# Kernel optimization log

Hardware: AMD Instinct MI355X
Metric: run time of the kernel (lower is better)

Reference implementation:

```python
import jax, jax.numpy as jnp
import numpy as np

K = 20  # number of top neighbors kept per row
NOISE_SCALE = 1e-4


def setup_inputs() -> dict:
    key = jax.random.key(0)
    k1, k2 = jax.random.split(key)
    B, N = 16, 2048
    A = jax.random.normal(k1, (B, N, N), dtype=jnp.float32)
    noise = jax.random.uniform(k2, (B, N, N), dtype=jnp.float32)
    return {"A": A, "noise": noise}


def reference(A, noise):
    # _activate: ReLU
    A = jax.nn.relu(A)

    # _sparsify: per-row top-k on noise-doped scores, scatter a 0/1 mask, multiply
    A_doped = A + noise * NOISE_SCALE
    _, topk_idx = jax.lax.top_k(A_doped, K)  # (B, N, K)
    B, N, _ = A.shape
    b_idx = jnp.arange(B)[:, None, None]
    r_idx = jnp.arange(N)[None, :, None]
    mask = jnp.zeros_like(A).at[b_idx, r_idx, topk_idx].set(1.0)
    A = A * mask

    # _symmetrize
    A = (A + jnp.swapaxes(A, 1, 2)) * 0.5

    # _normalize ('sym'): A <- D^{-1/2} (A + I) D^{-1/2}
    A = A + jnp.eye(N, dtype=A.dtype)
    d_inv = jnp.sum(A, axis=2) ** -0.5  # (B, N)
    d_inv = jnp.where(jnp.isinf(d_inv), 0.0, d_inv)
    # diag(d) @ A @ diag(d) expressed via broadcasting (same math as batched matmul)
    A = d_inv[:, :, None] * A * d_inv[:, None, :]
    return A
```

## Files before the change

### kernel.cpp

```cpp
#include <hip/hip_runtime.h>

#define NN 2048
#define KK 20
#define BB 16
#define T0F 1.8f
#define CAP 128
#define CSLOT 64

__global__ __launch_bounds__(256) void topk_kernel(
    const float* __restrict__ A, const float* __restrict__ noise,
    int* __restrict__ sel_idx, float* __restrict__ sel_val,
    float* __restrict__ colsum, int* __restrict__ col_cnt,
    unsigned short* __restrict__ col_src)
{
    __shared__ float cand_key[4][CAP];
    __shared__ float cand_val[4][CAP];
    __shared__ int   cand_idx[4][CAP];
    __shared__ int   tie_idx[4][64];
    __shared__ int   tie_cnt[4];

    const int lane = threadIdx.x & 63;
    const int wv   = threadIdx.x >> 6;
    const int row  = blockIdx.x * 4 + wv;
    const float* Ar = A     + (size_t)row * NN;
    const float* Nr = noise + (size_t)row * NN;
    const int colbase = row & ~(NN - 1);
    const unsigned long long ltm = (1ull << lane) - 1ull;

    int*   si = sel_idx + (size_t)row * KK;
    float* sv = sel_val + (size_t)row * KK;

    float key[32], val[32];
#pragma unroll
    for (int c = 0; c < 8; ++c) {
        float4 a4 = *(const float4*)(Ar + c * 256 + lane * 4);
        float4 n4 = *(const float4*)(Nr + c * 256 + lane * 4);
        val[c*4+0] = fmaxf(a4.x, 0.f); key[c*4+0] = val[c*4+0] + n4.x * 1e-4f;
        val[c*4+1] = fmaxf(a4.y, 0.f); key[c*4+1] = val[c*4+1] + n4.y * 1e-4f;
        val[c*4+2] = fmaxf(a4.z, 0.f); key[c*4+2] = val[c*4+2] + n4.z * 1e-4f;
        val[c*4+3] = fmaxf(a4.w, 0.f); key[c*4+3] = val[c*4+3] + n4.w * 1e-4f;
    }

#define EMIT(POS, IDX, V)                                                      \
    do {                                                                       \
        int _p = (POS); int _i = (IDX); float _v = (V);                        \
        si[_p] = _i; sv[_p] = _v;                                              \
        atomicAdd(&colsum[colbase + _i], _v);                                  \
        int _s = atomicAdd(&col_cnt[colbase + _i], 1);                         \
        if (_s < CSLOT)                                                        \
            col_src[(size_t)(colbase + _i) * CSLOT + _s] =                     \
                (unsigned short)(((row & (NN - 1)) << 5) | _p);                \
    } while (0)

    int cnt = 0;
#pragma unroll
    for (int j = 0; j < 32; ++j) {
        bool p = key[j] >= T0F;
        unsigned long long m = __ballot(p);
        if (p) {
            int pos = cnt + __popcll(m & ltm);
            if (pos < CAP) {
                cand_key[wv][pos] = key[j];
                cand_val[wv][pos] = val[j];
                cand_idx[wv][pos] = (j >> 2) * 256 + lane * 4 + (j & 3);
            }
        }
        cnt += __popcll(m);
    }

    bool done = false;
    if (cnt == KK) {
        if (lane < KK)
            EMIT(lane, cand_idx[wv][lane], cand_val[wv][lane]);
        done = true;
    } else if (cnt > KK && cnt <= CAP) {
        float c0 = (lane      < cnt) ? cand_key[wv][lane]      : -1.f;
        float c1 = (lane + 64 < cnt) ? cand_key[wv][lane + 64] : -1.f;

        float mx = fmaxf(c0, c1);
#pragma unroll
        for (int s = 32; s; s >>= 1) mx = fmaxf(mx, __shfl_xor(mx, s));

        unsigned lo = __float_as_uint(T0F);
        unsigned hi = __float_as_uint(mx) + 1u;
        bool exact = false; unsigned tb = 0;
        while (hi - lo > 1u) {
            unsigned mid = (lo + hi) >> 1;
            float tm = __uint_as_float(mid);
            int c = __popcll(__ballot(c0 >= tm)) + __popcll(__ballot(c1 >= tm));
            if (c == KK) { tb = mid; exact = true; break; }
            if (c > KK) lo = mid; else hi = mid;
        }
        if (exact) {
            float t = __uint_as_float(tb);
            bool p = c0 >= t;
            unsigned long long m = __ballot(p);
            if (p) EMIT(__popcll(m & ltm), cand_idx[wv][lane], cand_val[wv][lane]);
            int run = __popcll(m);
            p = c1 >= t;
            m = __ballot(p);
            if (p) EMIT(run + __popcll(m & ltm), cand_idx[wv][lane + 64],
                        cand_val[wv][lane + 64]);
            done = true;
        }
    }

    if (!done) {
        unsigned lo = 0u, hi = 0x7F800000u;
        unsigned tb = 0u;
        bool exact = false;
        while (hi - lo > 1u) {
            unsigned mid = (lo + hi) >> 1;
            float tm = __uint_as_float(mid);
            int c = 0;
#pragma unroll
            for (int j = 0; j < 32; ++j)
                c += __popcll(__ballot(key[j] >= tm));
            if (c == KK) { tb = mid; exact = true; break; }
            if (c > KK) lo = mid; else hi = mid;
        }
        if (exact) {
            float t = __uint_as_float(tb);
            int run = 0;
#pragma unroll
            for (int j = 0; j < 32; ++j) {
                bool p = key[j] >= t;
                unsigned long long m = __ballot(p);
                if (p) {
                    int pos = run + __popcll(m & ltm);
                    EMIT(pos, (j >> 2) * 256 + lane * 4 + (j & 3), val[j]);
                }
                run += __popcll(m);
            }
        } else {
            float t1 = __uint_as_float(lo);
            int run = 0;
#pragma unroll
            for (int j = 0; j < 32; ++j) {
                bool p = key[j] > t1;
                unsigned long long m = __ballot(p);
                if (p) {
                    int pos = run + __popcll(m & ltm);
                    EMIT(pos, (j >> 2) * 256 + lane * 4 + (j & 3), val[j]);
                }
                run += __popcll(m);
            }
            if (lane == 0) tie_cnt[wv] = 0;
#pragma unroll
            for (int j = 0; j < 32; ++j) {
                if (key[j] == t1) {
                    int p = atomicAdd(&tie_cnt[wv], 1);
                    if (p < 64) tie_idx[wv][p] = (j >> 2) * 256 + lane * 4 + (j & 3);
                }
            }
            if (lane == 0) {
                int n = tie_cnt[wv]; if (n > 64) n = 64;
                int need = KK - run;
                for (int s = 0; s < need; ++s) {
                    int bq = 0, bidx = 0x7fffffff;
                    for (int q = 0; q < n; ++q) {
                        int v = tie_idx[wv][q];
                        if (v < bidx) { bidx = v; bq = q; }
                    }
                    tie_idx[wv][bq] = 0x7fffffff;
                    float v = fmaxf(Ar[bidx], 0.f);
                    EMIT(run + s, bidx, v);
                }
            }
        }
    }
#undef EMIT
}

__global__ __launch_bounds__(256) void dinv_kernel(
    const float* __restrict__ sel_val, const float* __restrict__ colsum,
    float* __restrict__ dinv)
{
    int r = blockIdx.x * 256 + threadIdx.x;
    const float* svp = sel_val + (size_t)r * KK;
    float rs = 0.f;
#pragma unroll
    for (int k = 0; k < KK; ++k) rs += svp[k];
    float d = 1.0f + 0.5f * (rs + colsum[r]);
    dinv[r] = 1.0f / sqrtf(d);
}

__global__ __launch_bounds__(256) void dense_row_kernel(
    const int* __restrict__ sel_idx, const float* __restrict__ sel_val,
    const int* __restrict__ col_cnt, const unsigned short* __restrict__ col_src,
    const float* __restrict__ dinv, float* __restrict__ out)
{
    __shared__ float rowbuf[NN];
    const int r = blockIdx.x;
    const int i = r & (NN - 1);
    const int t = threadIdx.x;
    const int colbase = r & ~(NN - 1);

    float4 z = {0.f, 0.f, 0.f, 0.f};
#pragma unroll
    for (int c = 0; c < 2; ++c)
        *(float4*)(rowbuf + c * 1024 + t * 4) = z;
    __syncthreads();

    float di = dinv[r];
    if (t == 0) atomicAdd(&rowbuf[i], di * di);
    if (t < KK) {
        int j  = sel_idx[(size_t)r * KK + t];
        float v = sel_val[(size_t)r * KK + t];
        atomicAdd(&rowbuf[j], 0.5f * v * di * dinv[colbase + j]);
    }
    int cnt = col_cnt[r]; if (cnt > CSLOT) cnt = CSLOT;
    if (t < cnt) {
        unsigned short pk = col_src[(size_t)r * CSLOT + t];
        int srow = pk >> 5, k = pk & 31;
        float v = sel_val[(size_t)(colbase + srow) * KK + k];
        atomicAdd(&rowbuf[srow], 0.5f * v * di * dinv[colbase + srow]);
    }
    __syncthreads();

    size_t base = (size_t)r * NN;
#pragma unroll
    for (int c = 0; c < 2; ++c) {
        int col = c * 1024 + t * 4;
        *(float4*)(out + base + col) = *(const float4*)(rowbuf + col);
    }
}

extern "C" void kernel_launch(void* const* d_in, const int* in_sizes, int n_in,
                              void* d_out, int out_size, void* d_ws, size_t ws_size,
                              hipStream_t stream)
{
    const float* A     = (const float*)d_in[0];
    const float* noise = (const float*)d_in[1];
    float* out = (float*)d_out;
    char*  ws  = (char*)d_ws;

    const int rows = BB * NN;
    size_t off = 0;
    int*   sel_idx = (int*)(ws + off);            off += (size_t)rows * KK * 4;
    float* sel_val = (float*)(ws + off);          off += (size_t)rows * KK * 4;
    float* colsum  = (float*)(ws + off);          off += (size_t)rows * 4;
    float* dinv    = (float*)(ws + off);          off += (size_t)rows * 4;
    int*   col_cnt = (int*)(ws + off);            off += (size_t)rows * 4;
    unsigned short* col_src = (unsigned short*)(ws + off);

    hipMemsetAsync(colsum, 0, rows * sizeof(float), stream);
    hipMemsetAsync(col_cnt, 0, rows * sizeof(int), stream);

    topk_kernel<<<rows / 4, 256, 0, stream>>>(A, noise, sel_idx, sel_val,
                                              colsum, col_cnt, col_src);
    dinv_kernel<<<rows / 256, 256, 0, stream>>>(sel_val, colsum, dinv);
    dense_row_kernel<<<rows, 256, 0, stream>>>(sel_idx, sel_val, col_cnt,
                                               col_src, dinv, out);
}
```

Baseline: 636.8 us.

## Drop per-thread key/val arrays, reload rows in fallback path, use nontemporal stores

The top-k kernel no longer keeps 64 precomputed key/value registers per thread. It issues all raw loads up front, computes keys on the fly during candidate filtering, and re-reads A and noise from global memory in the rare binary-search fallback path. A launch-bounds occupancy hint of 4 is added to lower register pressure and raise occupancy. The dense output writes switch to nontemporal stores to avoid polluting cache. The fallback path changes element ordering (j*64+lane), so the order of tied picks may differ.

After: 700.8 us. 1.1x slower.

```diff
diff --git a/kernel.cpp b/kernel.cpp
--- a/kernel.cpp
+++ b/kernel.cpp
@@ -7,7 +7,9 @@
 #define CAP 128
 #define CSLOT 64
 
-__global__ __launch_bounds__(256) void topk_kernel(
+typedef __attribute__((ext_vector_type(4))) float f32x4;
+
+__global__ __launch_bounds__(256, 4) void topk_kernel(
     const float* __restrict__ A, const float* __restrict__ noise,
     int* __restrict__ sel_idx, float* __restrict__ sel_val,
     float* __restrict__ colsum, int* __restrict__ col_cnt,
@@ -29,17 +31,6 @@
 
     int*   si = sel_idx + (size_t)row * KK;
     float* sv = sel_val + (size_t)row * KK;
-
-    float key[32], val[32];
-#pragma unroll
-    for (int c = 0; c < 8; ++c) {
-        float4 a4 = *(const float4*)(Ar + c * 256 + lane * 4);
-        float4 n4 = *(const float4*)(Nr + c * 256 + lane * 4);
-        val[c*4+0] = fmaxf(a4.x, 0.f); key[c*4+0] = val[c*4+0] + n4.x * 1e-4f;
-        val[c*4+1] = fmaxf(a4.y, 0.f); key[c*4+1] = val[c*4+1] + n4.y * 1e-4f;
-        val[c*4+2] = fmaxf(a4.z, 0.f); key[c*4+2] = val[c*4+2] + n4.z * 1e-4f;
-        val[c*4+3] = fmaxf(a4.w, 0.f); key[c*4+3] = val[c*4+3] + n4.w * 1e-4f;
-    }
 
 #define EMIT(POS, IDX, V)                                                      \
     do {                                                                       \
@@ -52,20 +43,33 @@
                 (unsigned short)(((row & (NN - 1)) << 5) | _p);                \
     } while (0)
 
+    float4 a[8], z[8];
+#pragma unroll
+    for (int c = 0; c < 8; ++c) a[c] = *(const float4*)(Ar + c * 256 + lane * 4);
+#pragma unroll
+    for (int c = 0; c < 8; ++c) z[c] = *(const float4*)(Nr + c * 256 + lane * 4);
+
     int cnt = 0;
 #pragma unroll
-    for (int j = 0; j < 32; ++j) {
-        bool p = key[j] >= T0F;
-        unsigned long long m = __ballot(p);
-        if (p) {
-            int pos = cnt + __popcll(m & ltm);
-            if (pos < CAP) {
-                cand_key[wv][pos] = key[j];
-                cand_val[wv][pos] = val[j];
-                cand_idx[wv][pos] = (j >> 2) * 256 + lane * 4 + (j & 3);
-            }
-        }
-        cnt += __popcll(m);
+    for (int c = 0; c < 8; ++c) {
+        float av[4] = {a[c].x, a[c].y, a[c].z, a[c].w};
+        float nv[4] = {z[c].x, z[c].y, z[c].z, z[c].w};
+#pragma unroll
+        for (int q = 0; q < 4; ++q) {
+            float v = fmaxf(av[q], 0.f);
+            float k = v + nv[q] * 1e-4f;
+            bool p = k >= T0F;
+            unsigned long long m = __ballot(p);
+            if (p) {
+                int pos = cnt + __popcll(m & ltm);
+                if (pos < CAP) {
+                    cand_key[wv][pos] = k;
+                    cand_val[wv][pos] = v;
+                    cand_idx[wv][pos] = c * 256 + lane * 4 + q;
+                }
+            }
+            cnt += __popcll(m);
+        }
     }
 
     bool done = false;
@@ -113,44 +117,49 @@
             unsigned mid = (lo + hi) >> 1;
             float tm = __uint_as_float(mid);
             int c = 0;
-#pragma unroll
-            for (int j = 0; j < 32; ++j)
-                c += __popcll(__ballot(key[j] >= tm));
+            for (int j = 0; j < 32; ++j) {
+                float av = Ar[j * 64 + lane];
+                float nv = Nr[j * 64 + lane];
+                float k = fmaxf(av, 0.f) + nv * 1e-4f;
+                c += __popcll(__ballot(k >= tm));
+            }
             if (c == KK) { tb = mid; exact = true; break; }
             if (c > KK) lo = mid; else hi = mid;
         }
         if (exact) {
             float t = __uint_as_float(tb);
             int run = 0;
-#pragma unroll
-            for (int j = 0; j < 32; ++j) {
-                bool p = key[j] >= t;
+            for (int j = 0; j < 32; ++j) {
+                float av = Ar[j * 64 + lane];
+                float nv = Nr[j * 64 + lane];
+                float v = fmaxf(av, 0.f);
+                float k = v + nv * 1e-4f;
+                bool p = k >= t;
                 unsigned long long m = __ballot(p);
-                if (p) {
-                    int pos = run + __popcll(m & ltm);
-                    EMIT(pos, (j >> 2) * 256 + lane * 4 + (j & 3), val[j]);
-                }
+                if (p) EMIT(run + __popcll(m & ltm), j * 64 + lane, v);
                 run += __popcll(m);
             }
         } else {
             float t1 = __uint_as_float(lo);
             int run = 0;
-#pragma unroll
-            for (int j = 0; j < 32; ++j) {
-                bool p = key[j] > t1;
+            for (int j = 0; j < 32; ++j) {
+                float av = Ar[j * 64 + lane];
+                float nv = Nr[j * 64 + lane];
+                float v = fmaxf(av, 0.f);
+                float k = v + nv * 1e-4f;
+                bool p = k > t1;
                 unsigned long long m = __ballot(p);
-                if (p) {
-                    int pos = run + __popcll(m & ltm);
-                    EMIT(pos, (j >> 2) * 256 + lane * 4 + (j & 3), val[j]);
-                }
+                if (p) EMIT(run + __popcll(m & ltm), j * 64 + lane, v);
                 run += __popcll(m);
             }
             if (lane == 0) tie_cnt[wv] = 0;
-#pragma unroll
-            for (int j = 0; j < 32; ++j) {
-                if (key[j] == t1) {
+            for (int j = 0; j < 32; ++j) {
+                float av = Ar[j * 64 + lane];
+                float nv = Nr[j * 64 + lane];
+                float k = fmaxf(av, 0.f) + nv * 1e-4f;
+                if (k == t1) {
                     int p = atomicAdd(&tie_cnt[wv], 1);
-                    if (p < 64) tie_idx[wv][p] = (j >> 2) * 256 + lane * 4 + (j & 3);
+                    if (p < 64) tie_idx[wv][p] = j * 64 + lane;
                 }
             }
             if (lane == 0) {
@@ -196,10 +205,10 @@
     const int t = threadIdx.x;
     const int colbase = r & ~(NN - 1);
 
-    float4 z = {0.f, 0.f, 0.f, 0.f};
+    float4 zz = {0.f, 0.f, 0.f, 0.f};
 #pragma unroll
     for (int c = 0; c < 2; ++c)
-        *(float4*)(rowbuf + c * 1024 + t * 4) = z;
+        *(float4*)(rowbuf + c * 1024 + t * 4) = zz;
     __syncthreads();
 
     float di = dinv[r];
@@ -222,7 +231,8 @@
 #pragma unroll
     for (int c = 0; c < 2; ++c) {
         int col = c * 1024 + t * 4;
-        *(float4*)(out + base + col) = *(const float4*)(rowbuf + col);
+        f32x4 v = *(const f32x4*)(rowbuf + col);
+        __builtin_nontemporal_store(v, (f32x4*)(out + base + col));
     }
 }
 
```
